# Performance work log

Hardware: AMD Instinct MI355X
Metric: run time of the kernel (lower is better)

Reference implementation:

```python
import jax, jax.numpy as jnp
import numpy as np

FEATURE_DIM = 1024
N_CONCEPTS = 32768
BATCH = 1024
TEMPERATURE = 0.1
EPS = 1e-12  # matches torch F.normalize eps


def l2_normalize(x, axis=-1):
    n = jnp.linalg.norm(x, axis=axis, keepdims=True)
    return x / jnp.maximum(n, EPS)


def setup_inputs() -> dict:
    key = jax.random.key(0)
    k1, k2, k3, k4 = jax.random.split(key, 4)
    features = jax.random.normal(k1, (BATCH, FEATURE_DIM), dtype=jnp.float32)
    # Linear projection params (original inits to identity/zeros; random exercises the math)
    W = jnp.eye(FEATURE_DIM, dtype=jnp.float32) + 0.02 * jax.random.normal(k2, (FEATURE_DIM, FEATURE_DIM), dtype=jnp.float32)
    b = 0.01 * jax.random.normal(k3, (FEATURE_DIM,), dtype=jnp.float32)
    prototypes = l2_normalize(jax.random.normal(k4, (N_CONCEPTS, FEATURE_DIM), dtype=jnp.float32))
    return {"features": features, "W": W, "b": b, "prototypes": prototypes}


def reference(features, W, b, prototypes):
    # projection: features @ W.T + b   (torch nn.Linear convention)
    projected = jnp.einsum('bd,ed->be', features, W) + b          # [B, D]
    projected = l2_normalize(projected)                           # [B, D]
    # cosine similarity against all prototypes
    similarities = jnp.einsum('bd,kd->bk', projected, prototypes) # [B, K]
    activations = jax.nn.softmax(similarities / TEMPERATURE, axis=-1)
    best_idx = jnp.argmax(similarities, axis=-1)                  # [B] int
    return activations, best_idx
```

## Files before the change

kernel.cpp:

```cpp
#include <hip/hip_runtime.h>
#include <hip/hip_bf16.h>


typedef __attribute__((ext_vector_type(8))) short short8;
typedef __attribute__((ext_vector_type(4))) float floatx4;

__device__ __forceinline__ unsigned short f2bf(float f) {
  unsigned int u = __float_as_uint(f);
  u += 0x7fffu + ((u >> 16) & 1u);
  return (unsigned short)(u >> 16);
}
__device__ __forceinline__ float bf2f(unsigned short h) {
  return __uint_as_float(((unsigned int)h) << 16);
}

__global__ __launch_bounds__(256) void prep_convert(
    const float* __restrict__ protos, unsigned short* __restrict__ protoB,
    const float* __restrict__ features, unsigned short* __restrict__ Fh,
    unsigned short* __restrict__ Fm, unsigned short* __restrict__ Fl,
    const float* __restrict__ W, unsigned short* __restrict__ Wh,
    unsigned short* __restrict__ Wm, unsigned short* __restrict__ Wl) {
  const int blk = blockIdx.x;
  if (blk < 16384) {
    int i = blk * 256 + threadIdx.x;
    const float4* s4 = (const float4*)protos;
    float4 a = s4[2 * i];
    float4 b = s4[2 * i + 1];
    short8 o;
    o[0] = (short)f2bf(a.x); o[1] = (short)f2bf(a.y);
    o[2] = (short)f2bf(a.z); o[3] = (short)f2bf(a.w);
    o[4] = (short)f2bf(b.x); o[5] = (short)f2bf(b.y);
    o[6] = (short)f2bf(b.z); o[7] = (short)f2bf(b.w);
    ((short8*)protoB)[i] = o;
    return;
  }
  const float* src; unsigned short *H, *Md, *L; int i;
  if (blk < 17408) {
    src = features; H = Fh; Md = Fm; L = Fl;
    i = (blk - 16384) * 256 + threadIdx.x;
  } else {
    src = W; H = Wh; Md = Wm; L = Wl;
    i = (blk - 17408) * 256 + threadIdx.x;
  }
  float4 x = ((const float4*)src)[i];
  ushort4 h, m, l;
  float v, r;
  v = x.x; h.x = f2bf(v); r = v - bf2f(h.x); m.x = f2bf(r); l.x = f2bf(r - bf2f(m.x));
  v = x.y; h.y = f2bf(v); r = v - bf2f(h.y); m.y = f2bf(r); l.y = f2bf(r - bf2f(m.y));
  v = x.z; h.z = f2bf(v); r = v - bf2f(h.z); m.z = f2bf(r); l.z = f2bf(r - bf2f(m.z));
  v = x.w; h.w = f2bf(v); r = v - bf2f(h.w); m.w = f2bf(r); l.w = f2bf(r - bf2f(m.w));
  ((ushort4*)H)[i] = h; ((ushort4*)Md)[i] = m; ((ushort4*)L)[i] = l;
}


#define BARRIER() asm volatile("s_barrier" ::: "memory")
#define WAITLGKM()                                        \
  do {                                                    \
    asm volatile("s_waitcnt lgkmcnt(0)" ::: "memory");    \
    __builtin_amdgcn_sched_barrier(0);                    \
  } while (0)
#define WAITVM4() asm volatile("s_waitcnt vmcnt(4)" ::: "memory")

#define STAGE(OP, SLOT, H, KT)                                                 \
  do {                                                                         \
    const unsigned short* _s0 = (OP ? pB0 : pA0) + (H)*131072 + (KT)*64;       \
    const unsigned short* _s1 = (OP ? pB1 : pA1) + (H)*131072 + (KT)*64;       \
    __builtin_amdgcn_global_load_lds(                                          \
        (const __attribute__((address_space(1))) void*)_s0,                    \
        (__attribute__((address_space(3))) void*)(&lds[SLOT][OP][(H)*8192 + w * 512]), \
        16, 0, 0);                                                             \
    __builtin_amdgcn_global_load_lds(                                          \
        (const __attribute__((address_space(1))) void*)_s1,                    \
        (__attribute__((address_space(3))) void*)(&lds[SLOT][OP][(H)*8192 + 4096 + w * 512]), \
        16, 0, 0);                                                             \
  } while (0)

#define READ4(dst, base, off, rowadd)                                          \
  _Pragma("unroll") for (int q = 0; q < 4; q++)                                \
      dst[q] = *(const short8*)((base) + (off) + ((rowadd) + q) * 2048);

#define MFMA16(AB, BB, MBASE)                                                  \
  do {                                                                         \
    __builtin_amdgcn_sched_barrier(0);                                         \
    __builtin_amdgcn_s_setprio(1);                                             \
    _Pragma("unroll") for (int mf = 0; mf < 4; mf++)                           \
        _Pragma("unroll") for (int nf = 0; nf < 4; nf++)                       \
            acc[(MBASE) + mf][nf] = __builtin_amdgcn_mfma_f32_16x16x32_bf16(   \
                AB[mf], BB[nf], acc[(MBASE) + mf][nf], 0, 0, 0);               \
    __builtin_amdgcn_s_setprio(0);                                             \
    __builtin_amdgcn_sched_barrier(0);                                         \
  } while (0)

__global__ __launch_bounds__(512, 2) void gemm_nt_bf16_256(
    const unsigned short* __restrict__ A, const unsigned short* __restrict__ B,
    unsigned short* __restrict__ Cb, int M, int N, int K) {
  __shared__ unsigned short lds[2][2][16384];
  const int tid = threadIdx.x;
  const int w = tid >> 6, lane = tid & 63;
  const int wr = w >> 2, wc = w & 3;
  const int fr = lane & 15, koff8 = lane >> 4;

  const int bid = blockIdx.x;
  const int c8 = bid & 7, u = bid >> 3;
  const int nb = c8 * 16 + (u >> 2);
  const long tn = (long)nb * 256;
  const long tm = (long)(u & 3) * 256;

  const int idx0 = w * 64 + lane;
  const int idx1 = 512 + idx0;
  const int rh0 = idx0 >> 3, sc0 = (idx0 & 7) ^ (rh0 & 7);
  const int rh1 = idx1 >> 3, sc1 = (idx1 & 7) ^ (rh1 & 7);
  const unsigned short* pA0 = A + (tm + rh0) * 1024 + sc0 * 8;
  const unsigned short* pA1 = A + (tm + rh1) * 1024 + sc1 * 8;
  const unsigned short* pB0 = B + (tn + rh0) * 1024 + sc0 * 8;
  const unsigned short* pB1 = B + (tn + rh1) * 1024 + sc1 * 8;

  const int rA = wr * 128 + fr;
  const int rB = wc * 64 + fr;
  const int offA0 = rA * 128 + ((koff8 ^ (rA & 7)) << 4);
  const int offA1 = rA * 128 + (((koff8 ^ 4) ^ (rA & 7)) << 4);
  const int offB0 = rB * 128 + ((koff8 ^ (rB & 7)) << 4);
  const int offB1 = rB * 128 + (((koff8 ^ 4) ^ (rB & 7)) << 4);

  const char* ldsc = (const char*)&lds[0][0][0];
#define LDSA(s) (ldsc + (s)*65536)
#define LDSB(s) (ldsc + (s)*65536 + 32768)

  floatx4 acc[8][4];
#pragma unroll
  for (int i = 0; i < 8; i++)
#pragma unroll
    for (int j = 0; j < 4; j++) acc[i][j] = (floatx4){0.f, 0.f, 0.f, 0.f};

  short8 a0[4], a1[4], a2[4], b0[4], b1[4];

  STAGE(0, 0, 0, 0); STAGE(0, 0, 1, 0); STAGE(1, 0, 0, 0); STAGE(1, 0, 1, 0);
  STAGE(0, 1, 0, 1); STAGE(0, 1, 1, 1);
  WAITVM4();
  BARRIER();

#pragma unroll 1
  for (int i = 0; i < 8; i++) {
    const int t1 = 2 * i + 1;
    const int t2 = (2 * i + 2) & 15;
    const int t3 = (2 * i + 3) & 15;

    READ4(a0, LDSA(0), offA0, 0);
    READ4(a1, LDSA(0), offA0, 4);
    READ4(b0, LDSB(0), offB0, 0);
    STAGE(1, 1, 0, t1);
    BARRIER(); WAITLGKM();
    MFMA16(a0, b0, 0);
    BARRIER();
    READ4(a0, LDSA(0), offA1, 0);
    READ4(a2, LDSA(0), offA1, 4);
    READ4(b1, LDSB(0), offB1, 0);
    STAGE(1, 1, 1, t1);
    BARRIER(); WAITLGKM();
    MFMA16(a1, b0, 4);
    BARRIER();
    STAGE(0, 0, 0, t2);
    BARRIER();
    MFMA16(a0, b1, 0);
    BARRIER();
    STAGE(0, 0, 1, t2);
    WAITVM4();
    BARRIER();
    MFMA16(a2, b1, 4);
    BARRIER();

    READ4(a0, LDSA(1), offA0, 0);
    READ4(a1, LDSA(1), offA0, 4);
    READ4(b0, LDSB(1), offB0, 0);
    STAGE(1, 0, 0, t2);
    BARRIER(); WAITLGKM();
    MFMA16(a0, b0, 0);
    BARRIER();
    READ4(a0, LDSA(1), offA1, 0);
    READ4(a2, LDSA(1), offA1, 4);
    READ4(b1, LDSB(1), offB1, 0);
    STAGE(1, 0, 1, t2);
    BARRIER(); WAITLGKM();
    MFMA16(a1, b0, 4);
    BARRIER();
    STAGE(0, 1, 0, t3);
    BARRIER();
    MFMA16(a0, b1, 0);
    BARRIER();
    STAGE(0, 1, 1, t3);
    WAITVM4();
    BARRIER();
    MFMA16(a2, b1, 4);
    BARRIER();
  }

  const long crow = tm + wr * 128 + ((lane >> 4) * 4);
  const long ccol = tn + wc * 64 + fr;
  const long rs2 = 2 * (long)N;
#pragma unroll
  for (int mf = 0; mf < 8; mf++)
#pragma unroll
    for (int nf = 0; nf < 4; nf++)
#pragma unroll
      for (int r = 0; r < 4; r++)
        Cb[(crow + mf * 16 + r) * rs2 + N + ccol + nf * 16] =
            f2bf(acc[mf][nf][r]);
#undef LDSA
#undef LDSB
}

__global__ __launch_bounds__(256) void gemm_split6_nt(
    const unsigned short* __restrict__ Ah, const unsigned short* __restrict__ Am,
    const unsigned short* __restrict__ Al, const unsigned short* __restrict__ Bh,
    const unsigned short* __restrict__ Bm, const unsigned short* __restrict__ Bl,
    float* __restrict__ Cpart, float* __restrict__ Cpart2, int M, int N, int K) {
  __shared__ unsigned short sA[3][64 * 32];
  __shared__ unsigned short sB[3][64 * 32];
  const int tid  = threadIdx.x;
  const int wave = tid >> 6;
  const int lane = tid & 63;
  const long tm = (long)blockIdx.y * 64;
  const long tn = (long)blockIdx.x * 64;
  const int wm = (wave & 1) * 32;
  const int wn = (wave >> 1) * 32;
  const int ksize = K / gridDim.z;
  const int kbase = blockIdx.z * ksize;
  float* C = (blockIdx.z < 2) ? (Cpart + (size_t)blockIdx.z * M * N)
                              : (Cpart2 + (size_t)(blockIdx.z - 2) * M * N);

  floatx4 accH[2][2], accL[2][2];
#pragma unroll
  for (int i = 0; i < 2; i++)
#pragma unroll
    for (int j = 0; j < 2; j++) {
      accH[i][j] = (floatx4){0.f, 0.f, 0.f, 0.f};
      accL[i][j] = (floatx4){0.f, 0.f, 0.f, 0.f};
    }

  const int rstage = tid >> 2;
  const int cstage = (tid & 3) * 8;
  const long aoff = (tm + rstage) * (long)K + cstage;
  const long boff = (tn + rstage) * (long)K + cstage;
  const unsigned short* Asrc[3] = {Ah + aoff, Am + aoff, Al + aoff};
  const unsigned short* Bsrc[3] = {Bh + boff, Bm + boff, Bl + boff};

  for (int k0 = kbase; k0 < kbase + ksize; k0 += 32) {
#pragma unroll
    for (int p = 0; p < 3; p++) {
      __builtin_amdgcn_global_load_lds(
          (const __attribute__((address_space(1))) void*)(Asrc[p] + k0),
          (__attribute__((address_space(3))) void*)(sA[p] + wave * 512), 16, 0, 0);
      __builtin_amdgcn_global_load_lds(
          (const __attribute__((address_space(1))) void*)(Bsrc[p] + k0),
          (__attribute__((address_space(3))) void*)(sB[p] + wave * 512), 16, 0, 0);
    }
    __syncthreads();

    const int fr = lane & 15;
    const int koff = (lane >> 4) * 8;
    short8 a_[3][2], b_[3][2];
#pragma unroll
    for (int p = 0; p < 3; p++)
#pragma unroll
      for (int mf = 0; mf < 2; mf++) {
        a_[p][mf] = *(const short8*)(sA[p] + (wm + mf * 16 + fr) * 32 + koff);
        b_[p][mf] = *(const short8*)(sB[p] + (wn + mf * 16 + fr) * 32 + koff);
      }
#pragma unroll
    for (int mf = 0; mf < 2; mf++)
#pragma unroll
      for (int nf = 0; nf < 2; nf++) {
        accH[mf][nf] = __builtin_amdgcn_mfma_f32_16x16x32_bf16(
            a_[0][mf], b_[0][nf], accH[mf][nf], 0, 0, 0);
        accL[mf][nf] = __builtin_amdgcn_mfma_f32_16x16x32_bf16(
            a_[0][mf], b_[1][nf], accL[mf][nf], 0, 0, 0);
        accL[mf][nf] = __builtin_amdgcn_mfma_f32_16x16x32_bf16(
            a_[1][mf], b_[0][nf], accL[mf][nf], 0, 0, 0);
        accL[mf][nf] = __builtin_amdgcn_mfma_f32_16x16x32_bf16(
            a_[0][mf], b_[2][nf], accL[mf][nf], 0, 0, 0);
        accL[mf][nf] = __builtin_amdgcn_mfma_f32_16x16x32_bf16(
            a_[2][mf], b_[0][nf], accL[mf][nf], 0, 0, 0);
        accL[mf][nf] = __builtin_amdgcn_mfma_f32_16x16x32_bf16(
            a_[1][mf], b_[1][nf], accL[mf][nf], 0, 0, 0);
      }
    __syncthreads();
  }

  const long crow = tm + wm + ((lane >> 4) * 4);
  const long ccol = tn + wn + (lane & 15);
#pragma unroll
  for (int mf = 0; mf < 2; mf++)
#pragma unroll
    for (int nf = 0; nf < 2; nf++)
#pragma unroll
      for (int r = 0; r < 4; r++)
        C[(crow + mf * 16 + r) * (long)N + ccol + nf * 16] =
            accH[mf][nf][r] + accL[mf][nf][r];
}

__global__ __launch_bounds__(256) void norm_bias_rows(
    const float* __restrict__ P0, const float* __restrict__ P1,
    const float* __restrict__ Q, int nparts,
    const float* __restrict__ bias, unsigned short* __restrict__ Pn,
    float* __restrict__ Pn32) {
  const int b = blockIdx.x, tid = threadIdx.x;
  const long ro = (long)b * 1024;
  float4 v = ((const float4*)(P0 + ro))[tid];
  if (nparts == 8) {
    float4 t;
    t = ((const float4*)(P1 + ro))[tid];
    v.x += t.x; v.y += t.y; v.z += t.z; v.w += t.w;
#pragma unroll
    for (int z = 0; z < 6; z++) {
      t = ((const float4*)(Q + (size_t)z * 1024 * 1024 + ro))[tid];
      v.x += t.x; v.y += t.y; v.z += t.z; v.w += t.w;
    }
  }
  float4 bb = ((const float4*)bias)[tid];
  v.x += bb.x; v.y += bb.y; v.z += bb.z; v.w += bb.w;
  float ss = v.x * v.x + v.y * v.y + v.z * v.z + v.w * v.w;
#pragma unroll
  for (int off = 32; off > 0; off >>= 1) ss += __shfl_down(ss, off);
  __shared__ float wred[4];
  if ((tid & 63) == 0) wred[tid >> 6] = ss;
  __syncthreads();
  float tot = wred[0] + wred[1] + wred[2] + wred[3];
  float inv = 1.0f / fmaxf(sqrtf(tot), 1e-12f);
  float4 p = make_float4(v.x * inv, v.y * inv, v.z * inv, v.w * inv);
  ((float4*)Pn32)[b * 256 + tid] = p;
  ushort4 o;
  o.x = f2bf(p.x); o.y = f2bf(p.y); o.z = f2bf(p.z); o.w = f2bf(p.w);
  ((ushort4*)Pn)[b * 256 + tid] = o;
}

__global__ __launch_bounds__(256) void softmax_argmax_reg(
    float* __restrict__ out, const float* __restrict__ Pn32,
    const float* __restrict__ protos, float* __restrict__ idx_out) {
  const int b = blockIdx.x, tid = threadIdx.x;
  const int wave = tid >> 6, lane = tid & 63;
  __shared__ float sm_[4], sl_[4];
  __shared__ int cand[64];
  __shared__ int ncand;
  if (tid == 0) ncand = 0;

  const short8* src8 =
      (const short8*)((const char*)out + (size_t)b * 131072 + 65536);
  short8 v[16];
#pragma unroll
  for (int j = 0; j < 16; j++) v[j] = src8[tid + 256 * j];

  float m = -3.4e38f, l = 0.f;
#pragma unroll
  for (int j = 0; j < 16; j++) {
    float z0 = bf2f((unsigned short)v[j][0]) * 10.f;
    float z1 = bf2f((unsigned short)v[j][1]) * 10.f;
    float z2 = bf2f((unsigned short)v[j][2]) * 10.f;
    float z3 = bf2f((unsigned short)v[j][3]) * 10.f;
    float z4 = bf2f((unsigned short)v[j][4]) * 10.f;
    float z5 = bf2f((unsigned short)v[j][5]) * 10.f;
    float z6 = bf2f((unsigned short)v[j][6]) * 10.f;
    float z7 = bf2f((unsigned short)v[j][7]) * 10.f;
    float m8 = fmaxf(fmaxf(fmaxf(z0, z1), fmaxf(z2, z3)),
                     fmaxf(fmaxf(z4, z5), fmaxf(z6, z7)));
    float nm = fmaxf(m, m8);
    float s = __expf(z0 - nm) + __expf(z1 - nm) + __expf(z2 - nm) +
              __expf(z3 - nm) + __expf(z4 - nm) + __expf(z5 - nm) +
              __expf(z6 - nm) + __expf(z7 - nm);
    l = l * __expf(m - nm) + s;
    m = nm;
  }
#pragma unroll
  for (int off = 1; off < 64; off <<= 1) {
    float mo = __shfl_xor(m, off);
    float lo = __shfl_xor(l, off);
    float nm = fmaxf(m, mo);
    l = l * __expf(m - nm) + lo * __expf(mo - nm);
    m = nm;
  }
  if (lane == 0) { sm_[wave] = m; sl_[wave] = l; }
  __syncthreads();
  const float Mz = fmaxf(fmaxf(sm_[0], sm_[1]), fmaxf(sm_[2], sm_[3]));
  const float L = sl_[0] * __expf(sm_[0] - Mz) + sl_[1] * __expf(sm_[1] - Mz) +
                  sl_[2] * __expf(sm_[2] - Mz) + sl_[3] * __expf(sm_[3] - Mz);
  const float invL = 1.0f / L;
  const float thr = Mz * 0.1f - 0.016f;

  float* orow = out + (long)b * 32768;
#pragma unroll
  for (int j = 0; j < 16; j++) {
    const int i8 = tid + 256 * j;
    float s0 = bf2f((unsigned short)v[j][0]);
    float s1 = bf2f((unsigned short)v[j][1]);
    float s2 = bf2f((unsigned short)v[j][2]);
    float s3 = bf2f((unsigned short)v[j][3]);
    float s4 = bf2f((unsigned short)v[j][4]);
    float s5 = bf2f((unsigned short)v[j][5]);
    float s6 = bf2f((unsigned short)v[j][6]);
    float s7 = bf2f((unsigned short)v[j][7]);
    float mx = fmaxf(fmaxf(fmaxf(s0, s1), fmaxf(s2, s3)),
                     fmaxf(fmaxf(s4, s5), fmaxf(s6, s7)));
    if (mx >= thr) {
      if (s0 >= thr) { int p = atomicAdd(&ncand, 1); if (p < 64) cand[p] = i8 * 8 + 0; }
      if (s1 >= thr) { int p = atomicAdd(&ncand, 1); if (p < 64) cand[p] = i8 * 8 + 1; }
      if (s2 >= thr) { int p = atomicAdd(&ncand, 1); if (p < 64) cand[p] = i8 * 8 + 2; }
      if (s3 >= thr) { int p = atomicAdd(&ncand, 1); if (p < 64) cand[p] = i8 * 8 + 3; }
      if (s4 >= thr) { int p = atomicAdd(&ncand, 1); if (p < 64) cand[p] = i8 * 8 + 4; }
      if (s5 >= thr) { int p = atomicAdd(&ncand, 1); if (p < 64) cand[p] = i8 * 8 + 5; }
      if (s6 >= thr) { int p = atomicAdd(&ncand, 1); if (p < 64) cand[p] = i8 * 8 + 6; }
      if (s7 >= thr) { int p = atomicAdd(&ncand, 1); if (p < 64) cand[p] = i8 * 8 + 7; }
    }
    float4 e0, e1;
    e0.x = __expf(s0 * 10.f - Mz) * invL;
    e0.y = __expf(s1 * 10.f - Mz) * invL;
    e0.z = __expf(s2 * 10.f - Mz) * invL;
    e0.w = __expf(s3 * 10.f - Mz) * invL;
    e1.x = __expf(s4 * 10.f - Mz) * invL;
    e1.y = __expf(s5 * 10.f - Mz) * invL;
    e1.z = __expf(s6 * 10.f - Mz) * invL;
    e1.w = __expf(s7 * 10.f - Mz) * invL;
    ((float4*)orow)[2 * i8] = e0;
    ((float4*)orow)[2 * i8 + 1] = e1;
  }
  __syncthreads();
  int n = ncand < 64 ? ncand : 64;

  float4 pv = ((const float4*)(Pn32 + (long)b * 1024))[tid];
  __shared__ double dred[4];
  double best = -1e300;
  int besti = 0x7fffffff;
  for (int c = 0; c < n; c++) {
    int k = cand[c];
    float4 kv = ((const float4*)(protos + (long)k * 1024))[tid];
    double d = (double)pv.x * kv.x + (double)pv.y * kv.y +
               (double)pv.z * kv.z + (double)pv.w * kv.w;
#pragma unroll
    for (int off = 32; off > 0; off >>= 1) d += __shfl_down(d, off);
    if (lane == 0) dred[wave] = d;
    __syncthreads();
    if (tid == 0) {
      double tot = dred[0] + dred[1] + dred[2] + dred[3];
      if (tot > best || (tot == best && k < besti)) { best = tot; besti = k; }
    }
    __syncthreads();
  }
  if (tid == 0) idx_out[b] = (float)besti;
}

extern "C" void kernel_launch(void* const* d_in, const int* in_sizes, int n_in,
                              void* d_out, int out_size, void* d_ws, size_t ws_size,
                              hipStream_t stream) {
  const float* features = (const float*)d_in[0];
  const float* W        = (const float*)d_in[1];
  const float* bias     = (const float*)d_in[2];
  const float* protos   = (const float*)d_in[3];

  const size_t MB = 1024 * 1024;
  char* ws = (char*)d_ws;
  unsigned short* protoB = (unsigned short*)ws;
  unsigned short* Fh = (unsigned short*)(ws + 64 * MB);
  unsigned short* Fm = (unsigned short*)(ws + 66 * MB);
  unsigned short* Fl = (unsigned short*)(ws + 68 * MB);
  unsigned short* Wh = (unsigned short*)(ws + 70 * MB);
  unsigned short* Wm = (unsigned short*)(ws + 72 * MB);
  unsigned short* Wl = (unsigned short*)(ws + 74 * MB);
  float*          P0 = (float*)(ws + 76 * MB);
  float*          P1 = (float*)(ws + 80 * MB);
  float*          Q  = (float*)d_out;
  unsigned short* Pn   = (unsigned short*)(ws + 64 * MB);
  float*          Pn32 = (float*)(ws + 66 * MB);

  const int ksplit = (ws_size >= 84 * MB) ? 8 : 1;

  float* S = (float*)d_out;
  float* idx_out = S + (size_t)1024 * 32768;

  prep_convert<<<18432, 256, 0, stream>>>(protos, protoB, features, Fh, Fm, Fl,
                                          W, Wh, Wm, Wl);
  gemm_split6_nt<<<dim3(16, 16, ksplit), 256, 0, stream>>>(
      Fh, Fm, Fl, Wh, Wm, Wl, P0, Q, 1024, 1024, 1024);
  norm_bias_rows<<<1024, 256, 0, stream>>>(P0, P1, Q, ksplit, bias, Pn, Pn32);
  gemm_nt_bf16_256<<<512, 512, 0, stream>>>(Pn, protoB, (unsigned short*)d_out,
                                            1024, 32768, 1024);
  softmax_argmax_reg<<<1024, 256, 0, stream>>>(S, Pn32, protos, idx_out);
}
```

Before: 419.1 us.

## Split row softmax/argmax into chunked partial-reduce, activation, and refine kernels

The single per-row softmax+argmax kernel (one 256-thread block per row, each holding a large register array) is split into three kernels. Eight blocks per row compute partial max/sum, then eight blocks per row apply the normalized exp and collect argmax candidates through global atomics, and a final per-row kernel refines the argmax in double precision. The GEMM epilogue now places the bf16 similarities at the start of each 4096-column chunk's own output region, so each chunk block reads its data before overwriting it with floats. This is meant to raise occupancy and parallelism in the memory-bound tail. In exchange it re-reads the bf16 scores, adds two kernel launches and moves candidate-list traffic to global memory.

```diff
diff --git a/kernel.cpp b/kernel.cpp
--- a/kernel.cpp
+++ b/kernel.cpp
@@ -195,7 +195,8 @@
   }
 
   const long crow = tm + wr * 128 + ((lane >> 4) * 4);
-  const long ccol = tn + wc * 64 + fr;
+  const int cb = ((int)(tn >> 12)) * 8192;
+  const int scol = ((int)tn & 4095) + wc * 64 + fr;
   const long rs2 = 2 * (long)N;
 #pragma unroll
   for (int mf = 0; mf < 8; mf++)
@@ -203,7 +204,7 @@
     for (int nf = 0; nf < 4; nf++)
 #pragma unroll
       for (int r = 0; r < 4; r++)
-        Cb[(crow + mf * 16 + r) * rs2 + N + ccol + nf * 16] =
+        Cb[(crow + mf * 16 + r) * rs2 + cb + scol + nf * 16] =
             f2bf(acc[mf][nf][r]);
 #undef LDSA
 #undef LDSB
@@ -333,42 +334,43 @@
   ((ushort4*)Pn)[b * 256 + tid] = o;
 }
 
-__global__ __launch_bounds__(256) void softmax_argmax_reg(
-    float* __restrict__ out, const float* __restrict__ Pn32,
-    const float* __restrict__ protos, float* __restrict__ idx_out) {
-  const int b = blockIdx.x, tid = threadIdx.x;
+
+__global__ __launch_bounds__(256) void row_ml_part(
+    const float* __restrict__ out, float2* __restrict__ mlp,
+    int* __restrict__ ncand) {
+  const int bid = blockIdx.x;
+  const int row = bid >> 3, chunk = bid & 7, tid = threadIdx.x;
   const int wave = tid >> 6, lane = tid & 63;
-  __shared__ float sm_[4], sl_[4];
-  __shared__ int cand[64];
-  __shared__ int ncand;
-  if (tid == 0) ncand = 0;
-
-  const short8* src8 =
-      (const short8*)((const char*)out + (size_t)b * 131072 + 65536);
-  short8 v[16];
-#pragma unroll
-  for (int j = 0; j < 16; j++) v[j] = src8[tid + 256 * j];
-
-  float m = -3.4e38f, l = 0.f;
-#pragma unroll
-  for (int j = 0; j < 16; j++) {
-    float z0 = bf2f((unsigned short)v[j][0]) * 10.f;
-    float z1 = bf2f((unsigned short)v[j][1]) * 10.f;
-    float z2 = bf2f((unsigned short)v[j][2]) * 10.f;
-    float z3 = bf2f((unsigned short)v[j][3]) * 10.f;
-    float z4 = bf2f((unsigned short)v[j][4]) * 10.f;
-    float z5 = bf2f((unsigned short)v[j][5]) * 10.f;
-    float z6 = bf2f((unsigned short)v[j][6]) * 10.f;
-    float z7 = bf2f((unsigned short)v[j][7]) * 10.f;
-    float m8 = fmaxf(fmaxf(fmaxf(z0, z1), fmaxf(z2, z3)),
-                     fmaxf(fmaxf(z4, z5), fmaxf(z6, z7)));
-    float nm = fmaxf(m, m8);
-    float s = __expf(z0 - nm) + __expf(z1 - nm) + __expf(z2 - nm) +
-              __expf(z3 - nm) + __expf(z4 - nm) + __expf(z5 - nm) +
-              __expf(z6 - nm) + __expf(z7 - nm);
-    l = l * __expf(m - nm) + s;
-    m = nm;
-  }
+  if (chunk == 0 && tid == 0) ncand[row] = 0;
+  const short8* src8 = (const short8*)((const char*)out +
+                                       (size_t)row * 131072 +
+                                       (size_t)chunk * 16384);
+  short8 v0 = src8[tid];
+  short8 v1 = src8[tid + 256];
+
+  float z0 = bf2f((unsigned short)v0[0]) * 10.f;
+  float z1 = bf2f((unsigned short)v0[1]) * 10.f;
+  float z2 = bf2f((unsigned short)v0[2]) * 10.f;
+  float z3 = bf2f((unsigned short)v0[3]) * 10.f;
+  float z4 = bf2f((unsigned short)v0[4]) * 10.f;
+  float z5 = bf2f((unsigned short)v0[5]) * 10.f;
+  float z6 = bf2f((unsigned short)v0[6]) * 10.f;
+  float z7 = bf2f((unsigned short)v0[7]) * 10.f;
+  float y0 = bf2f((unsigned short)v1[0]) * 10.f;
+  float y1 = bf2f((unsigned short)v1[1]) * 10.f;
+  float y2 = bf2f((unsigned short)v1[2]) * 10.f;
+  float y3 = bf2f((unsigned short)v1[3]) * 10.f;
+  float y4 = bf2f((unsigned short)v1[4]) * 10.f;
+  float y5 = bf2f((unsigned short)v1[5]) * 10.f;
+  float y6 = bf2f((unsigned short)v1[6]) * 10.f;
+  float y7 = bf2f((unsigned short)v1[7]) * 10.f;
+  float m = fmaxf(
+      fmaxf(fmaxf(fmaxf(z0, z1), fmaxf(z2, z3)), fmaxf(fmaxf(z4, z5), fmaxf(z6, z7))),
+      fmaxf(fmaxf(fmaxf(y0, y1), fmaxf(y2, y3)), fmaxf(fmaxf(y4, y5), fmaxf(y6, y7))));
+  float l = __expf(z0 - m) + __expf(z1 - m) + __expf(z2 - m) + __expf(z3 - m) +
+            __expf(z4 - m) + __expf(z5 - m) + __expf(z6 - m) + __expf(z7 - m) +
+            __expf(y0 - m) + __expf(y1 - m) + __expf(y2 - m) + __expf(y3 - m) +
+            __expf(y4 - m) + __expf(y5 - m) + __expf(y6 - m) + __expf(y7 - m);
 #pragma unroll
   for (int off = 1; off < 64; off <<= 1) {
     float mo = __shfl_xor(m, off);
@@ -377,37 +379,67 @@
     l = l * __expf(m - nm) + lo * __expf(mo - nm);
     m = nm;
   }
+  __shared__ float sm_[4], sl_[4];
   if (lane == 0) { sm_[wave] = m; sl_[wave] = l; }
   __syncthreads();
-  const float Mz = fmaxf(fmaxf(sm_[0], sm_[1]), fmaxf(sm_[2], sm_[3]));
-  const float L = sl_[0] * __expf(sm_[0] - Mz) + sl_[1] * __expf(sm_[1] - Mz) +
-                  sl_[2] * __expf(sm_[2] - Mz) + sl_[3] * __expf(sm_[3] - Mz);
+  if (tid == 0) {
+    float Mb = fmaxf(fmaxf(sm_[0], sm_[1]), fmaxf(sm_[2], sm_[3]));
+    float Lb = sl_[0] * __expf(sm_[0] - Mb) + sl_[1] * __expf(sm_[1] - Mb) +
+               sl_[2] * __expf(sm_[2] - Mb) + sl_[3] * __expf(sm_[3] - Mb);
+    mlp[bid] = make_float2(Mb, Lb);
+  }
+}
+
+__global__ __launch_bounds__(256) void act_cand(
+    float* __restrict__ out, const float2* __restrict__ mlp,
+    int* __restrict__ ncand, int* __restrict__ candlist) {
+  const int bid = blockIdx.x;
+  const int row = bid >> 3, chunk = bid & 7, tid = threadIdx.x;
+
+  float2 q0 = mlp[row * 8 + 0], q1 = mlp[row * 8 + 1];
+  float2 q2 = mlp[row * 8 + 2], q3 = mlp[row * 8 + 3];
+  float2 q4 = mlp[row * 8 + 4], q5 = mlp[row * 8 + 5];
+  float2 q6 = mlp[row * 8 + 6], q7 = mlp[row * 8 + 7];
+  const float Mz = fmaxf(fmaxf(fmaxf(q0.x, q1.x), fmaxf(q2.x, q3.x)),
+                         fmaxf(fmaxf(q4.x, q5.x), fmaxf(q6.x, q7.x)));
+  const float L = q0.y * __expf(q0.x - Mz) + q1.y * __expf(q1.x - Mz) +
+                  q2.y * __expf(q2.x - Mz) + q3.y * __expf(q3.x - Mz) +
+                  q4.y * __expf(q4.x - Mz) + q5.y * __expf(q5.x - Mz) +
+                  q6.y * __expf(q6.x - Mz) + q7.y * __expf(q7.x - Mz);
   const float invL = 1.0f / L;
   const float thr = Mz * 0.1f - 0.016f;
 
-  float* orow = out + (long)b * 32768;
-#pragma unroll
-  for (int j = 0; j < 16; j++) {
-    const int i8 = tid + 256 * j;
-    float s0 = bf2f((unsigned short)v[j][0]);
-    float s1 = bf2f((unsigned short)v[j][1]);
-    float s2 = bf2f((unsigned short)v[j][2]);
-    float s3 = bf2f((unsigned short)v[j][3]);
-    float s4 = bf2f((unsigned short)v[j][4]);
-    float s5 = bf2f((unsigned short)v[j][5]);
-    float s6 = bf2f((unsigned short)v[j][6]);
-    float s7 = bf2f((unsigned short)v[j][7]);
+  const short8* src8 = (const short8*)((const char*)out +
+                                       (size_t)row * 131072 +
+                                       (size_t)chunk * 16384);
+  short8 v0 = src8[tid];
+  short8 v1 = src8[tid + 256];
+  __syncthreads();
+
+  float* orow = out + (long)row * 32768;
+#pragma unroll
+  for (int j = 0; j < 2; j++) {
+    const int i8 = chunk * 512 + tid + 256 * j;
+    short8 v = (j == 0) ? v0 : v1;
+    float s0 = bf2f((unsigned short)v[0]);
+    float s1 = bf2f((unsigned short)v[1]);
+    float s2 = bf2f((unsigned short)v[2]);
+    float s3 = bf2f((unsigned short)v[3]);
+    float s4 = bf2f((unsigned short)v[4]);
+    float s5 = bf2f((unsigned short)v[5]);
+    float s6 = bf2f((unsigned short)v[6]);
+    float s7 = bf2f((unsigned short)v[7]);
     float mx = fmaxf(fmaxf(fmaxf(s0, s1), fmaxf(s2, s3)),
                      fmaxf(fmaxf(s4, s5), fmaxf(s6, s7)));
     if (mx >= thr) {
-      if (s0 >= thr) { int p = atomicAdd(&ncand, 1); if (p < 64) cand[p] = i8 * 8 + 0; }
-      if (s1 >= thr) { int p = atomicAdd(&ncand, 1); if (p < 64) cand[p] = i8 * 8 + 1; }
-      if (s2 >= thr) { int p = atomicAdd(&ncand, 1); if (p < 64) cand[p] = i8 * 8 + 2; }
-      if (s3 >= thr) { int p = atomicAdd(&ncand, 1); if (p < 64) cand[p] = i8 * 8 + 3; }
-      if (s4 >= thr) { int p = atomicAdd(&ncand, 1); if (p < 64) cand[p] = i8 * 8 + 4; }
-      if (s5 >= thr) { int p = atomicAdd(&ncand, 1); if (p < 64) cand[p] = i8 * 8 + 5; }
-      if (s6 >= thr) { int p = atomicAdd(&ncand, 1); if (p < 64) cand[p] = i8 * 8 + 6; }
-      if (s7 >= thr) { int p = atomicAdd(&ncand, 1); if (p < 64) cand[p] = i8 * 8 + 7; }
+      if (s0 >= thr) { int p = atomicAdd(&ncand[row], 1); if (p < 64) candlist[row * 64 + p] = i8 * 8 + 0; }
+      if (s1 >= thr) { int p = atomicAdd(&ncand[row], 1); if (p < 64) candlist[row * 64 + p] = i8 * 8 + 1; }
+      if (s2 >= thr) { int p = atomicAdd(&ncand[row], 1); if (p < 64) candlist[row * 64 + p] = i8 * 8 + 2; }
+      if (s3 >= thr) { int p = atomicAdd(&ncand[row], 1); if (p < 64) candlist[row * 64 + p] = i8 * 8 + 3; }
+      if (s4 >= thr) { int p = atomicAdd(&ncand[row], 1); if (p < 64) candlist[row * 64 + p] = i8 * 8 + 4; }
+      if (s5 >= thr) { int p = atomicAdd(&ncand[row], 1); if (p < 64) candlist[row * 64 + p] = i8 * 8 + 5; }
+      if (s6 >= thr) { int p = atomicAdd(&ncand[row], 1); if (p < 64) candlist[row * 64 + p] = i8 * 8 + 6; }
+      if (s7 >= thr) { int p = atomicAdd(&ncand[row], 1); if (p < 64) candlist[row * 64 + p] = i8 * 8 + 7; }
     }
     float4 e0, e1;
     e0.x = __expf(s0 * 10.f - Mz) * invL;
@@ -421,15 +453,21 @@
     ((float4*)orow)[2 * i8] = e0;
     ((float4*)orow)[2 * i8 + 1] = e1;
   }
-  __syncthreads();
-  int n = ncand < 64 ? ncand : 64;
-
+}
+
+__global__ __launch_bounds__(256) void argmax_refine(
+    const int* __restrict__ ncand, const int* __restrict__ candlist,
+    const float* __restrict__ Pn32, const float* __restrict__ protos,
+    float* __restrict__ idx_out) {
+  const int b = blockIdx.x, tid = threadIdx.x;
+  const int wave = tid >> 6, lane = tid & 63;
+  int n = ncand[b]; n = n < 64 ? n : 64;
   float4 pv = ((const float4*)(Pn32 + (long)b * 1024))[tid];
   __shared__ double dred[4];
   double best = -1e300;
   int besti = 0x7fffffff;
   for (int c = 0; c < n; c++) {
-    int k = cand[c];
+    int k = candlist[b * 64 + c];
     float4 kv = ((const float4*)(protos + (long)k * 1024))[tid];
     double d = (double)pv.x * kv.x + (double)pv.y * kv.y +
                (double)pv.z * kv.z + (double)pv.w * kv.w;
@@ -468,6 +506,9 @@
   float*          Q  = (float*)d_out;
   unsigned short* Pn   = (unsigned short*)(ws + 64 * MB);
   float*          Pn32 = (float*)(ws + 66 * MB);
+  float2* mlp      = (float2*)(ws + 70 * MB);
+  int*    ncand    = (int*)(ws + 70 * MB + 128 * 1024);
+  int*    candlist = (int*)(ws + 70 * MB + 256 * 1024);
 
   const int ksplit = (ws_size >= 84 * MB) ? 8 : 1;
 
@@ -481,5 +522,8 @@
   norm_bias_rows<<<1024, 256, 0, stream>>>(P0, P1, Q, ksplit, bias, Pn, Pn32);
   gemm_nt_bf16_256<<<512, 512, 0, stream>>>(Pn, protoB, (unsigned short*)d_out,
                                             1024, 32768, 1024);
-  softmax_argmax_reg<<<1024, 256, 0, stream>>>(S, Pn32, protos, idx_out);
-}
+  row_ml_part<<<8192, 256, 0, stream>>>(S, mlp, ncand);
+  act_cand<<<8192, 256, 0, stream>>>(S, mlp, ncand, candlist);
+  argmax_refine<<<1024, 256, 0, stream>>>(ncand, candlist, Pn32, protos,
+                                          idx_out);
+}
```

New measurement: 409.6 us. 2.3% less time.
